# Performance work log

Measured on AMD Instinct MI355X. Metric: run time of the kernel, lower is better.

The kernel has to match this reference:

```python
import jax, jax.numpy as jnp
import numpy as np

N, D_IN, D_LAT, D_FEAT, K = 12000, 64, 16, 64, 16


def setup_inputs() -> dict:
    key = jax.random.key(0)
    ks = jax.random.split(key, 7)
    s_in = 1.0 / np.sqrt(D_IN)
    s_cat = 1.0 / np.sqrt(2 * D_FEAT)
    return {
        "x": jax.random.normal(ks[0], (N, D_IN), dtype=jnp.float32),
        "W_feat": jax.random.uniform(ks[1], (D_IN, D_FEAT), jnp.float32, -s_in, s_in),
        "b_feat": jax.random.uniform(ks[2], (D_FEAT,), jnp.float32, -s_in, s_in),
        "W_lat": jax.random.uniform(ks[3], (D_IN, D_LAT), jnp.float32, -s_in, s_in),
        "b_lat": jax.random.uniform(ks[4], (D_LAT,), jnp.float32, -s_in, s_in),
        "W_out": jax.random.uniform(ks[5], (2 * D_FEAT, D_FEAT), jnp.float32, -s_cat, s_cat),
        "b_out": jax.random.uniform(ks[6], (D_FEAT,), jnp.float32, -s_cat, s_cat),
    }


def reference(x, W_feat, b_feat, W_lat, b_lat, W_out, b_out):
    # dense encoders
    feats = jnp.tanh(x @ W_feat + b_feat)      # [N, F] learned features
    coords = jnp.tanh(x @ W_lat + b_lat)       # [N, S] latent coordinates
    n = coords.shape[0]
    # full pairwise squared euclidean distances (as the module's cdist)
    sq = jnp.sum(coords * coords, axis=1)
    d2 = sq[:, None] + sq[None, :] - 2.0 * (coords @ coords.T)   # [N, N]
    d2 = jnp.maximum(d2, 0.0)
    # knn_graph: k nearest neighbors, excluding self (loop=False)
    d2_masked = jnp.where(jnp.eye(n, dtype=bool), jnp.inf, d2)
    neg_d2, idx = jax.lax.top_k(-d2_masked, K)                   # idx: [N, K] neighbor (source) ids
    edge_d2 = -neg_d2                                            # squared dist to each neighbor
    # gaussian kernel on euclidean distance: w = exp(-d^2)
    w = jnp.exp(-edge_d2)                                        # [N, K]
    # message = w * x_j, aggr='add': out_i = sum_k w_ik * feats[idx_ik]
    agg = jnp.einsum('nk,nkf->nf', w, feats[idx])                # [N, F]
    # cat self features with aggregated messages, final dense
    out = jnp.concatenate([feats, agg], axis=1) @ W_out + b_out  # [N, F]
    return out
```

## Files before the change

### kernel.cpp

```cpp
#include <hip/hip_runtime.h>
#include <math.h>

typedef unsigned long long u64;
typedef _Float16 f16x8 __attribute__((ext_vector_type(8)));
typedef float f32x16 __attribute__((ext_vector_type(16)));

#define N_PTS 12000
#define KNN 16
#define QB 16
#define NWAVES 8
#define NGROUPS32 (N_PTS / 32)
#define TAU_PTS 2048
#define TAU_GROUPS32 (TAU_PTS / 32)
#define CAP 384
#define MARGIN 0.08f
#define EVICT_KEY ((u64)0x7F400000u << 32)

__global__ __launch_bounds__(256) void encoder_kernel(
    const float* __restrict__ x, const float* __restrict__ Wf, const float* __restrict__ bf,
    const float* __restrict__ Wl, const float* __restrict__ bl,
    float* __restrict__ feats, float* __restrict__ coords, _Float16* __restrict__ coords_h,
    float* __restrict__ sq)
{
  const int wave = threadIdx.x >> 6;
  const int lane = threadIdx.x & 63;
  const int i = blockIdx.x * 4 + wave;
  if (i >= N_PTS) return;
  float xv = x[i * 64 + lane];
  float accf = bf[lane];
  float accc = bl[lane & 15];
  #pragma unroll
  for (int k = 0; k < 64; ++k) {
    float xk = __shfl(xv, k);
    accf = fmaf(xk, Wf[k * 64 + lane], accf);
    accc = fmaf(xk, Wl[k * 16 + (lane & 15)], accc);
  }
  feats[i * 64 + lane] = tanhf(accf);
  float c = tanhf(accc);
  float cc = (lane < 16) ? c * c : 0.0f;
  cc += __shfl_xor(cc, 1);
  cc += __shfl_xor(cc, 2);
  cc += __shfl_xor(cc, 4);
  cc += __shfl_xor(cc, 8);
  if (lane < 16) {
    coords[i * 16 + lane] = c;
    coords_h[i * 16 + lane] = (_Float16)c;
  }
  if (lane == 0) sq[i] = cc;
}

__device__ __forceinline__ void ins6(u64 key, u64* k6, u64& kmax) {
  const u64 om = (key < kmax) ? kmax : ~0ull;
  #pragma unroll
  for (int t = 0; t < 6; ++t)
    k6[t] = (k6[t] == om) ? key : k6[t];
  u64 a = k6[0] > k6[1] ? k6[0] : k6[1];
  u64 b = k6[2] > k6[3] ? k6[2] : k6[3];
  u64 c = k6[4] > k6[5] ? k6[4] : k6[5];
  a = a > b ? a : b;
  kmax = a > c ? a : c;
}

__device__ __forceinline__ void ins8(u64 key, u64* k8, u64& kmax) {
  const u64 om = (key < kmax) ? kmax : ~0ull;
  #pragma unroll
  for (int t = 0; t < 8; ++t)
    k8[t] = (k8[t] == om) ? key : k8[t];
  u64 a = k8[0] > k8[1] ? k8[0] : k8[1];
  u64 b = k8[2] > k8[3] ? k8[2] : k8[3];
  u64 c = k8[4] > k8[5] ? k8[4] : k8[5];
  u64 d = k8[6] > k8[7] ? k8[6] : k8[7];
  a = a > b ? a : b;
  c = c > d ? c : d;
  kmax = a > c ? a : c;
}

__device__ __forceinline__ u64 shflx_u64(u64 v, int off) {
  int lo = __shfl_xor((int)(unsigned)v, off);
  int hi = __shfl_xor((int)(unsigned)(v >> 32), off);
  return ((u64)(unsigned)hi << 32) | (unsigned)lo;
}

__device__ __forceinline__ u64 minbfly(u64 m) {
  #pragma unroll
  for (int off = 32; off >= 1; off >>= 1) {
    u64 o = shflx_u64(m, off);
    m = (o < m) ? o : m;
  }
  return m;
}

__global__ __launch_bounds__(512) void knn_agg_kernel(
    const float* __restrict__ coords, const _Float16* __restrict__ coords_h,
    const float* __restrict__ sq, const float* __restrict__ feats,
    const float* __restrict__ Wo, const float* __restrict__ bo,
    float* __restrict__ out, int* __restrict__ flags)
{
  __shared__ unsigned short sbuf[QB][CAP];
  __shared__ int scnt[QB];
  __shared__ unsigned colminS[QB][64];
  __shared__ float taugS[QB];
  __shared__ float featS[QB][64];
  __shared__ float aggS[QB][64];

  const int tid = threadIdx.x;
  const int lane = tid & 63;
  const int wave = tid >> 6;
  const int qbase = blockIdx.x * QB;
  const int mcol = lane & 31;
  const int half = lane >> 5;

  if (tid < QB) scnt[tid] = 0;
  #pragma unroll
  for (int t = tid; t < QB * 64; t += 512)
    ((unsigned*)colminS)[t] = 0x7F800000u;

  f16x8 afrag = {0, 0, 0, 0, 0, 0, 0, 0};
  if (mcol < QB) {
    const uint4 u = *(const uint4*)((const char*)coords_h + (qbase + mcol) * 32 + half * 16);
    afrag = __builtin_bit_cast(f16x8, u);
  }
  float sqi8[8];
  #pragma unroll
  for (int blk = 0; blk < 2; ++blk) {
    const float4 v = *(const float4*)&sq[qbase + blk * 8 + 4 * half];
    sqi8[blk * 4 + 0] = v.x; sqi8[blk * 4 + 1] = v.y;
    sqi8[blk * 4 + 2] = v.z; sqi8[blk * 4 + 3] = v.w;
  }
  __syncthreads();

  float lmin8[8] = {INFINITY, INFINITY, INFINITY, INFINITY,
                    INFINITY, INFINITY, INFINITY, INFINITY};
  for (int g = wave; g < TAU_GROUPS32; g += NWAVES) {
    const int j0 = g * 32;
    const uint4 u = *(const uint4*)((const char*)coords_h + (j0 + mcol) * 32 + half * 16);
    const f16x8 bfrag = __builtin_bit_cast(f16x8, u);
    const float sqj = sq[j0 + mcol];
    f32x16 acc = {0.0f};
    acc = __builtin_amdgcn_mfma_f32_32x32x16_f16(afrag, bfrag, acc, 0, 0, 0);
    #pragma unroll
    for (int r = 0; r < 8; ++r) {
      const int row = (r >> 2) * 8 + 4 * half + (r & 3);
      float d2a = fmaf(-2.0f, acc[r], sqi8[r] + sqj);
      if (j0 + mcol == qbase + row) d2a = INFINITY;
      lmin8[r] = fminf(lmin8[r], d2a);
    }
  }
  {
    const int cell = mcol * 2 + (wave >> 2);
    #pragma unroll
    for (int r = 0; r < 8; ++r) {
      const int row = (r >> 2) * 8 + 4 * half + (r & 3);
      atomicMin(&colminS[row][cell], __float_as_uint(fmaxf(lmin8[r], 0.0f)));
    }
  }
  __syncthreads();

  #pragma unroll
  for (int s = 0; s < 2; ++s) {
    const int q = wave * 2 + s;
    float v = __uint_as_float(colminS[q][lane]);
    #pragma unroll
    for (int k = 2; k <= 64; k <<= 1) {
      #pragma unroll
      for (int st = k >> 1; st >= 1; st >>= 1) {
        const float o = __shfl_xor(v, st);
        const bool keepMin = (((lane & st) == 0) == ((lane & k) == 0));
        const float mn = fminf(v, o), mx = fmaxf(v, o);
        v = keepMin ? mn : mx;
      }
    }
    const float tq = __shfl(v, 15) + MARGIN;
    if (lane == 0) taugS[q] = tq;
  }
  __syncthreads();

  float thr8[8];
  #pragma unroll
  for (int r = 0; r < 8; ++r)
    thr8[r] = 0.5f * (sqi8[r] - taugS[(r >> 2) * 8 + 4 * half + (r & 3)]);

  for (int g = wave; g < NGROUPS32; g += NWAVES) {
    const int j0 = g * 32;
    const uint4 u = *(const uint4*)((const char*)coords_h + (j0 + mcol) * 32 + half * 16);
    const f16x8 bfrag = __builtin_bit_cast(f16x8, u);
    const float hs = 0.5f * sq[j0 + mcol];
    f32x16 acc = {0.0f};
    acc = __builtin_amdgcn_mfma_f32_32x32x16_f16(afrag, bfrag, acc, 0, 0, 0);
    #pragma unroll
    for (int r = 0; r < 8; ++r) {
      if (acc[r] >= thr8[r] + hs) {
        const int row = (r >> 2) * 8 + 4 * half + (r & 3);
        const int p = atomicAdd(&scnt[row], 1);
        if (p < CAP) sbuf[row][p] = (unsigned short)(j0 + mcol);
      }
    }
  }
  __syncthreads();

  #pragma unroll
  for (int s = 0; s < 2; ++s) {
    const int lq = wave * 2 + s;
    const int qg = qbase + lq;
    const int cq = scnt[lq];
    const int nread = (cq < CAP) ? cq : CAP;
    const int nit = (nread + 63) >> 6;

    float ci[16];
    {
      const float4* cp = (const float4*)(coords + qg * 16);
      *(float4*)&ci[0] = cp[0]; *(float4*)&ci[4] = cp[1];
      *(float4*)&ci[8] = cp[2]; *(float4*)&ci[12] = cp[3];
    }
    const float sqiq = sq[qg];

    u64 k6[6];
    #pragma unroll
    for (int t = 0; t < 6; ++t) k6[t] = ((u64)(0x7F000000u + t) << 32);
    u64 kmax6 = ((u64)0x7F000005u << 32);

    for (int t = 0; t < nit; ++t) {
      const int idx = t * 64 + lane;
      u64 key = ~0ull;
      if (idx < nread) {
        const int jj = sbuf[lq][idx];
        if (jj != qg) {
          const float4* cp = (const float4*)(coords + jj * 16);
          float cj[16];
          *(float4*)&cj[0]  = cp[0]; *(float4*)&cj[4]  = cp[1];
          *(float4*)&cj[8]  = cp[2]; *(float4*)&cj[12] = cp[3];
          float dot = 0.0f;
          #pragma unroll
          for (int d = 0; d < 16; ++d) dot = fmaf(ci[d], cj[d], dot);
          const float d2 = fmaxf(fmaf(-2.0f, dot, sqiq + sq[jj]), 0.0f);
          key = ((u64)__float_as_uint(d2) << 32) | (unsigned)jj;
        }
      }
      ins6(key, k6, kmax6);
    }

    u64 lmin = k6[0];
    #pragma unroll
    for (int t = 1; t < 6; ++t) lmin = (k6[t] < lmin) ? k6[t] : lmin;
    float dmin = __uint_as_float((unsigned)(lmin >> 32));
    int jmin = (int)(unsigned)(lmin & 0xFFFFFFFFull);

    float dv[16]; int jv[16];
    #pragma unroll
    for (int r = 0; r < KNN; ++r) {
      float m = dmin;
      #pragma unroll
      for (int off = 32; off >= 1; off >>= 1)
        m = fminf(m, __shfl_xor(m, off));
      const u64 bal = __ballot(dmin == m);
      const int owner = __ffsll((unsigned long long)bal) - 1;
      jv[r] = __builtin_amdgcn_readlane(jmin, owner);
      dv[r] = __uint_as_float(__builtin_amdgcn_readfirstlane(__float_as_uint(m)));
      if (lane == owner) {
        #pragma unroll
        for (int t = 0; t < 6; ++t)
          k6[t] = (k6[t] == lmin) ? EVICT_KEY : k6[t];
        lmin = k6[0];
        #pragma unroll
        for (int t = 1; t < 6; ++t) lmin = (k6[t] < lmin) ? k6[t] : lmin;
        dmin = __uint_as_float((unsigned)(lmin >> 32));
        jmin = (int)(unsigned)(lmin & 0xFFFFFFFFull);
      }
    }

    float aggv = 0.0f;
    #pragma unroll
    for (int r = 0; r < KNN; ++r)
      aggv = fmaf(expf(-dv[r]), feats[jv[r] * 64 + lane], aggv);

    aggS[lq][lane] = aggv;
    featS[lq][lane] = feats[qg * 64 + lane];
    if (lane == 0) flags[qg] = (cq > CAP);
  }

  __syncthreads();
  const int row = tid >> 5;
  const int c2 = (tid & 31) * 2;
  float acc0 = bo[c2], acc1 = bo[c2 + 1];
  #pragma unroll
  for (int f = 0; f < 64; ++f) {
    const float fv = featS[row][f];
    const float av = aggS[row][f];
    const float2 w0 = *(const float2*)&Wo[f * 64 + c2];
    const float2 w1 = *(const float2*)&Wo[(64 + f) * 64 + c2];
    acc0 = fmaf(fv, w0.x, acc0); acc0 = fmaf(av, w1.x, acc0);
    acc1 = fmaf(fv, w0.y, acc1); acc1 = fmaf(av, w1.y, acc1);
  }
  const int orow = qbase + row;
  *(float2*)&out[orow * 64 + c2] = make_float2(acc0, acc1);
}

__global__ __launch_bounds__(256) void knn_fixup_kernel(
    const float* __restrict__ coords, const float* __restrict__ sq,
    const float* __restrict__ feats, const int* __restrict__ flags,
    const float* __restrict__ Wo, const float* __restrict__ bo,
    float* __restrict__ out)
{
  const int wave = threadIdx.x >> 6;
  const int lane = threadIdx.x & 63;
  const int i = blockIdx.x * 4 + wave;
  if (i >= N_PTS) return;
  if (!flags[i]) return;
  float ci[16];
  #pragma unroll
  for (int d = 0; d < 16; ++d) ci[d] = coords[i * 16 + d];
  const float sqi = sq[i];

  u64 k8a[8], k8b[8], kmaxA, kmaxB;
  #pragma unroll
  for (int t = 0; t < 8; ++t) {
    k8a[t] = ((u64)(0x7F000000u + t) << 32);
    k8b[t] = ((u64)(0x7F000000u + t) << 32);
  }
  kmaxA = ((u64)0x7F000007u << 32);
  kmaxB = ((u64)0x7F000007u << 32);

  const int niter = (N_PTS + 63) / 64;
  for (int t = 0; t < niter; ++t) {
    const int j = t * 64 + lane;
    float4 c0 = make_float4(0,0,0,0), c1 = c0, c2 = c0, c3 = c0;
    float sqj = 0.0f;
    if (j < N_PTS) {
      const float4* cp = (const float4*)(coords + j * 16);
      c0 = cp[0]; c1 = cp[1]; c2 = cp[2]; c3 = cp[3];
      sqj = sq[j];
    }
    float dot = ci[0]*c0.x + ci[1]*c0.y + ci[2]*c0.z + ci[3]*c0.w
              + ci[4]*c1.x + ci[5]*c1.y + ci[6]*c1.z + ci[7]*c1.w
              + ci[8]*c2.x + ci[9]*c2.y + ci[10]*c2.z + ci[11]*c2.w
              + ci[12]*c3.x + ci[13]*c3.y + ci[14]*c3.z + ci[15]*c3.w;
    float d2 = fmaxf(fmaf(-2.0f, dot, sqi + sqj), 0.0f);
    const unsigned hi = (j == i || j >= N_PTS) ? 0xFFFFFFFFu : __float_as_uint(d2);
    const u64 key = ((u64)hi << 32) | (unsigned)j;
    if (t & 1) ins8(key, k8a, kmaxA);
    else       ins8(key, k8b, kmaxB);
  }

  u64 tab[16];
  #pragma unroll
  for (int t = 0; t < 8; ++t) { tab[t] = k8a[t]; tab[8 + t] = k8b[t]; }
  u64 lmin = tab[0];
  #pragma unroll
  for (int t = 1; t < 16; ++t) lmin = (tab[t] < lmin) ? tab[t] : lmin;

  float aggv = 0.0f;
  u64 T16 = 0;
  for (int r = 0; r < KNN; ++r) {
    const u64 m = minbfly(lmin);
    if (lmin == m) {
      #pragma unroll
      for (int t = 0; t < 16; ++t) tab[t] = (tab[t] == m) ? ~0ull : tab[t];
      lmin = tab[0];
      #pragma unroll
      for (int t = 1; t < 16; ++t) lmin = (tab[t] < lmin) ? tab[t] : lmin;
    }
    const unsigned hi = (unsigned)(m >> 32);
    const bool ok = hi < 0x7F000000u;
    const float w = ok ? expf(-__uint_as_float(hi)) : 0.0f;
    const int jj = ok ? (int)(unsigned)(m & 0xFFFFFFFFull) : 0;
    aggv = fmaf(w, feats[jj * 64 + lane], aggv);
    T16 = m;
  }

  if (__any((kmaxA < T16) || (kmaxB < T16))) {
    aggv = 0.0f;
    u64 prev = 0;
    for (int r = 0; r < KNN; ++r) {
      u64 best = ~0ull;
      for (int j = lane; j < N_PTS; j += 64) {
        float dot = 0.0f;
        #pragma unroll
        for (int d = 0; d < 16; ++d) dot = fmaf(ci[d], coords[j * 16 + d], dot);
        const float d2 = fmaxf(fmaf(-2.0f, dot, sqi + sq[j]), 0.0f);
        const unsigned hi = (j == i) ? 0xFFFFFFFFu : __float_as_uint(d2);
        const u64 key = ((u64)hi << 32) | (unsigned)j;
        const bool cand = (r == 0) || (key > prev);
        if (cand && key < best) best = key;
      }
      const u64 m = minbfly(best);
      prev = m;
      const unsigned hi = (unsigned)(m >> 32);
      const bool ok = hi < 0x7F000000u;
      const float w = ok ? expf(-__uint_as_float(hi)) : 0.0f;
      const int jj = ok ? (int)(unsigned)(m & 0xFFFFFFFFull) : 0;
      aggv = fmaf(w, feats[jj * 64 + lane], aggv);
    }
  }

  const float fl = feats[i * 64 + lane];
  float acc = bo[lane];
  #pragma unroll
  for (int f = 0; f < 64; ++f) {
    acc = fmaf(__shfl(fl, f),   Wo[f * 64 + lane],        acc);
    acc = fmaf(__shfl(aggv, f), Wo[(64 + f) * 64 + lane], acc);
  }
  out[i * 64 + lane] = acc;
}

extern "C" void kernel_launch(void* const* d_in, const int* in_sizes, int n_in,
                              void* d_out, int out_size, void* d_ws, size_t ws_size,
                              hipStream_t stream) {
  const float* x  = (const float*)d_in[0];
  const float* Wf = (const float*)d_in[1];
  const float* bf = (const float*)d_in[2];
  const float* Wl = (const float*)d_in[3];
  const float* bl = (const float*)d_in[4];
  const float* Wo = (const float*)d_in[5];
  const float* bo = (const float*)d_in[6];
  float* out = (float*)d_out;

  char* ws = (char*)d_ws;
  float*     feats    = (float*)(ws);
  float*     coords   = (float*)(ws + 3072000);
  float*     sqv      = (float*)(ws + 3840000);
  _Float16*  coords_h = (_Float16*)(ws + 3888000);
  int*       flags    = (int*)(ws + 4272000);

  encoder_kernel<<<3000, 256, 0, stream>>>(x, Wf, bf, Wl, bl, feats, coords, coords_h, sqv);
  knn_agg_kernel<<<N_PTS / QB, 512, 0, stream>>>(coords, coords_h, sqv, feats, Wo, bo, out, flags);
  knn_fixup_kernel<<<3000, 256, 0, stream>>>(coords, sqv, feats, flags, Wo, bo, out);
}
```

Measured before the change: 172.0 us.

## Fold distance offsets into MFMA accumulator, sort per-lane candidates, vectorize epilogue

Measured after the change: 174.3 us. Within noise of the previous version (+1.4%).

```diff
diff --git a/kernel.cpp b/kernel.cpp
--- a/kernel.cpp
+++ b/kernel.cpp
@@ -90,6 +90,9 @@
   return m;
 }
 
+#define CAS6(i, j) { const u64 a_ = k6[i], b_ = k6[j]; const bool sw_ = a_ > b_; \
+                     k6[i] = sw_ ? b_ : a_; k6[j] = sw_ ? a_ : b_; }
+
 __global__ __launch_bounds__(512) void knn_agg_kernel(
     const float* __restrict__ coords, const _Float16* __restrict__ coords_h,
     const float* __restrict__ sq, const float* __restrict__ feats,
@@ -100,8 +103,8 @@
   __shared__ int scnt[QB];
   __shared__ unsigned colminS[QB][64];
   __shared__ float taugS[QB];
-  __shared__ float featS[QB][64];
-  __shared__ float aggS[QB][64];
+  __shared__ __align__(16) float featS[QB][64];
+  __shared__ __align__(16) float aggS[QB][64];
 
   const int tid = threadIdx.x;
   const int lane = tid & 63;
@@ -120,38 +123,49 @@
     const uint4 u = *(const uint4*)((const char*)coords_h + (qbase + mcol) * 32 + half * 16);
     afrag = __builtin_bit_cast(f16x8, u);
   }
-  float sqi8[8];
+  float sqi8[8], nhsqi8[8];
   #pragma unroll
   for (int blk = 0; blk < 2; ++blk) {
     const float4 v = *(const float4*)&sq[qbase + blk * 8 + 4 * half];
     sqi8[blk * 4 + 0] = v.x; sqi8[blk * 4 + 1] = v.y;
     sqi8[blk * 4 + 2] = v.z; sqi8[blk * 4 + 3] = v.w;
   }
+  #pragma unroll
+  for (int r = 0; r < 8; ++r) nhsqi8[r] = -0.5f * sqi8[r];
+
+  f32x16 acc;
+  #pragma unroll
+  for (int t = 0; t < 16; ++t) acc[t] = 0.0f;
+
   __syncthreads();
 
-  float lmin8[8] = {INFINITY, INFINITY, INFINITY, INFINITY,
-                    INFINITY, INFINITY, INFINITY, INFINITY};
+  const int g_self = qbase >> 5;
+  float lmax8[8] = {-INFINITY, -INFINITY, -INFINITY, -INFINITY,
+                    -INFINITY, -INFINITY, -INFINITY, -INFINITY};
   for (int g = wave; g < TAU_GROUPS32; g += NWAVES) {
     const int j0 = g * 32;
     const uint4 u = *(const uint4*)((const char*)coords_h + (j0 + mcol) * 32 + half * 16);
     const f16x8 bfrag = __builtin_bit_cast(f16x8, u);
     const float sqj = sq[j0 + mcol];
-    f32x16 acc = {0.0f};
+    #pragma unroll
+    for (int r = 0; r < 8; ++r) acc[r] = fmaf(-0.5f, sqj, nhsqi8[r]);
     acc = __builtin_amdgcn_mfma_f32_32x32x16_f16(afrag, bfrag, acc, 0, 0, 0);
+    if (g == g_self) {
+      #pragma unroll
+      for (int r = 0; r < 8; ++r) {
+        const int row = (r >> 2) * 8 + 4 * half + (r & 3);
+        if (j0 + mcol == qbase + row) acc[r] = -INFINITY;
+      }
+    }
+    #pragma unroll
+    for (int r = 0; r < 8; ++r) lmax8[r] = fmaxf(lmax8[r], acc[r]);
+  }
+  {
+    const int cell = mcol * 2 + (wave >> 2);
     #pragma unroll
     for (int r = 0; r < 8; ++r) {
       const int row = (r >> 2) * 8 + 4 * half + (r & 3);
-      float d2a = fmaf(-2.0f, acc[r], sqi8[r] + sqj);
-      if (j0 + mcol == qbase + row) d2a = INFINITY;
-      lmin8[r] = fminf(lmin8[r], d2a);
-    }
-  }
-  {
-    const int cell = mcol * 2 + (wave >> 2);
-    #pragma unroll
-    for (int r = 0; r < 8; ++r) {
-      const int row = (r >> 2) * 8 + 4 * half + (r & 3);
-      atomicMin(&colminS[row][cell], __float_as_uint(fmaxf(lmin8[r], 0.0f)));
+      atomicMin(&colminS[row][cell], __float_as_uint(fmaxf(-2.0f * lmax8[r], 0.0f)));
     }
   }
   __syncthreads();
@@ -175,24 +189,29 @@
   }
   __syncthreads();
 
-  float thr8[8];
+  float nht8[8];
   #pragma unroll
   for (int r = 0; r < 8; ++r)
-    thr8[r] = 0.5f * (sqi8[r] - taugS[(r >> 2) * 8 + 4 * half + (r & 3)]);
-
+    nht8[r] = -0.5f * taugS[(r >> 2) * 8 + 4 * half + (r & 3)];
+
+  #pragma unroll 2
   for (int g = wave; g < NGROUPS32; g += NWAVES) {
     const int j0 = g * 32;
     const uint4 u = *(const uint4*)((const char*)coords_h + (j0 + mcol) * 32 + half * 16);
     const f16x8 bfrag = __builtin_bit_cast(f16x8, u);
-    const float hs = 0.5f * sq[j0 + mcol];
-    f32x16 acc = {0.0f};
+    const float sqj = sq[j0 + mcol];
+    #pragma unroll
+    for (int r = 0; r < 8; ++r) acc[r] = fmaf(-0.5f, sqj, nhsqi8[r]);
     acc = __builtin_amdgcn_mfma_f32_32x32x16_f16(afrag, bfrag, acc, 0, 0, 0);
     #pragma unroll
     for (int r = 0; r < 8; ++r) {
-      if (acc[r] >= thr8[r] + hs) {
-        const int row = (r >> 2) * 8 + 4 * half + (r & 3);
-        const int p = atomicAdd(&scnt[row], 1);
-        if (p < CAP) sbuf[row][p] = (unsigned short)(j0 + mcol);
+      const bool pass = acc[r] >= nht8[r];
+      if (__any(pass)) {
+        if (pass) {
+          const int row = (r >> 2) * 8 + 4 * half + (r & 3);
+          const int p = atomicAdd(&scnt[row], 1);
+          if (p < CAP) sbuf[row][p] = (unsigned short)(j0 + mcol);
+        }
       }
     }
   }
@@ -239,11 +258,14 @@
       ins6(key, k6, kmax6);
     }
 
-    u64 lmin = k6[0];
-    #pragma unroll
-    for (int t = 1; t < 6; ++t) lmin = (k6[t] < lmin) ? k6[t] : lmin;
-    float dmin = __uint_as_float((unsigned)(lmin >> 32));
-    int jmin = (int)(unsigned)(lmin & 0xFFFFFFFFull);
+    CAS6(0,5) CAS6(1,3) CAS6(2,4)
+    CAS6(1,2) CAS6(3,4)
+    CAS6(0,3) CAS6(2,5)
+    CAS6(0,1) CAS6(2,3) CAS6(4,5)
+    CAS6(1,2) CAS6(3,4)
+
+    float dmin = __uint_as_float((unsigned)(k6[0] >> 32));
+    int jmin = (int)(unsigned)(k6[0] & 0xFFFFFFFFull);
 
     float dv[16]; int jv[16];
     #pragma unroll
@@ -256,22 +278,21 @@
       const int owner = __ffsll((unsigned long long)bal) - 1;
       jv[r] = __builtin_amdgcn_readlane(jmin, owner);
       dv[r] = __uint_as_float(__builtin_amdgcn_readfirstlane(__float_as_uint(m)));
-      if (lane == owner) {
-        #pragma unroll
-        for (int t = 0; t < 6; ++t)
-          k6[t] = (k6[t] == lmin) ? EVICT_KEY : k6[t];
-        lmin = k6[0];
-        #pragma unroll
-        for (int t = 1; t < 6; ++t) lmin = (k6[t] < lmin) ? k6[t] : lmin;
-        dmin = __uint_as_float((unsigned)(lmin >> 32));
-        jmin = (int)(unsigned)(lmin & 0xFFFFFFFFull);
-      }
+      const bool me = (lane == owner);
+      k6[0] = me ? k6[1] : k6[0];
+      k6[1] = me ? k6[2] : k6[1];
+      k6[2] = me ? k6[3] : k6[2];
+      k6[3] = me ? k6[4] : k6[3];
+      k6[4] = me ? k6[5] : k6[4];
+      k6[5] = me ? EVICT_KEY : k6[5];
+      dmin = __uint_as_float((unsigned)(k6[0] >> 32));
+      jmin = (int)(unsigned)(k6[0] & 0xFFFFFFFFull);
     }
 
     float aggv = 0.0f;
     #pragma unroll
     for (int r = 0; r < KNN; ++r)
-      aggv = fmaf(expf(-dv[r]), feats[jv[r] * 64 + lane], aggv);
+      aggv = fmaf(__expf(-dv[r]), feats[jv[r] * 64 + lane], aggv);
 
     aggS[lq][lane] = aggv;
     featS[lq][lane] = feats[qg * 64 + lane];
@@ -283,13 +304,18 @@
   const int c2 = (tid & 31) * 2;
   float acc0 = bo[c2], acc1 = bo[c2 + 1];
   #pragma unroll
-  for (int f = 0; f < 64; ++f) {
-    const float fv = featS[row][f];
-    const float av = aggS[row][f];
-    const float2 w0 = *(const float2*)&Wo[f * 64 + c2];
-    const float2 w1 = *(const float2*)&Wo[(64 + f) * 64 + c2];
-    acc0 = fmaf(fv, w0.x, acc0); acc0 = fmaf(av, w1.x, acc0);
-    acc1 = fmaf(fv, w0.y, acc1); acc1 = fmaf(av, w1.y, acc1);
+  for (int f0 = 0; f0 < 64; f0 += 4) {
+    const float4 fv = *(const float4*)&featS[row][f0];
+    const float4 av = *(const float4*)&aggS[row][f0];
+    #pragma unroll
+    for (int u = 0; u < 4; ++u) {
+      const float fvu = (u == 0) ? fv.x : (u == 1) ? fv.y : (u == 2) ? fv.z : fv.w;
+      const float avu = (u == 0) ? av.x : (u == 1) ? av.y : (u == 2) ? av.z : av.w;
+      const float2 w0 = *(const float2*)&Wo[(f0 + u) * 64 + c2];
+      const float2 w1 = *(const float2*)&Wo[(64 + f0 + u) * 64 + c2];
+      acc0 = fmaf(fvu, w0.x, acc0); acc0 = fmaf(avu, w1.x, acc0);
+      acc1 = fmaf(fvu, w0.y, acc1); acc1 = fmaf(avu, w1.y, acc1);
+    }
   }
   const int orow = qbase + row;
   *(float2*)&out[orow * 64 + c2] = make_float2(acc0, acc1);
```
